# Performance work log

Hardware: AMD Instinct MI355X
Metric: run time of the kernel (lower is better)

The kernel has to match this reference:

```python
import jax, jax.numpy as jnp
import numpy as np

K_TOP = 16
TEMP = 1.0
EPS = 1e-9

def setup_inputs() -> dict:
    key = jax.random.key(0)
    k1, k2, k3 = jax.random.split(key, 3)
    B, H, N, D = 4, 8, 2048, 64
    q = jax.random.normal(k1, (B, H, N, D), dtype=jnp.float32)
    k = jax.random.normal(k2, (B, H, N, D), dtype=jnp.float32)
    u = jax.random.uniform(k3, (B, N, N), dtype=jnp.float32)
    return {"q": q, "k": k, "u": u}

def reference(q, k, u):
    # q, k: [B, H, N, D]; u: uniform noise [B, N, N]
    d_head = q.shape[-1]
    scale = 1.0 / jnp.sqrt(jnp.asarray(d_head, dtype=q.dtype))
    # [B, H, N, N] scores, then mean over heads -> [B, N, N]
    attn_scores = jnp.einsum('bhnd,bhmd->bhnm', q, k) * scale
    logits = attn_scores.mean(axis=1)
    gumbel = -jnp.log(-jnp.log(u + EPS) + EPS)
    probs = jax.nn.softmax((logits + gumbel) / TEMP, axis=-1)
    topk_vals = jax.lax.top_k(probs, K_TOP)[0]          # [B, N, K]
    thresh = topk_vals.min(axis=-1, keepdims=True)      # [B, N, 1]
    sparse_mask = (probs >= thresh).astype(probs.dtype)
    return sparse_mask[:, None, :, :]                   # [B, 1, N, N]
```

## Files before the change

### kernel.cpp

```cpp
#include <hip/hip_runtime.h>
#include <math.h>

#define BB 4
#define HH 8
#define NN 2048
#define DD 64
#define KTOP 16
#define CUT_MARGIN 1e-3f

typedef _Float16 half_t;
typedef __attribute__((ext_vector_type(8))) _Float16 half8;
typedef __attribute__((ext_vector_type(4))) _Float16 half4v;
typedef __attribute__((ext_vector_type(4))) float floatx4;

__global__ __launch_bounds__(256) void split_f16(const float* __restrict__ q,
                                                 const float* __restrict__ kk,
                                                 half_t* __restrict__ qhi,
                                                 half_t* __restrict__ qlo,
                                                 half_t* __restrict__ khi,
                                                 half_t* __restrict__ klo) {
    const int NQ4 = BB * HH * NN * DD / 4;
    int gid = blockIdx.x * 256 + threadIdx.x;
    const float* src; half_t* dhi; half_t* dlo; int i4;
    if (gid < NQ4) { src = q;  dhi = qhi; dlo = qlo; i4 = gid; }
    else           { src = kk; dhi = khi; dlo = klo; i4 = gid - NQ4; }
    float4 x = ((const float4*)src)[i4];
    float xs[4] = {x.x, x.y, x.z, x.w};
    half4v h, l;
#pragma unroll
    for (int e = 0; e < 4; ++e) {
        half_t hi = (half_t)xs[e];
        float  r  = xs[e] - (float)hi;
        h[e] = hi;
        l[e] = (half_t)(r * 2048.0f);
    }
    *(half4v*)(dhi + (size_t)i4 * 4) = h;
    *(half4v*)(dlo + (size_t)i4 * 4) = l;
}

__global__ __launch_bounds__(256, 2) void gemm_f16x3(const half_t* __restrict__ qhi,
                                                     const half_t* __restrict__ qlo,
                                                     const half_t* __restrict__ khi,
                                                     const half_t* __restrict__ klo,
                                                     float* __restrict__ L) {
    const int b  = blockIdx.z;
    const int i0 = blockIdx.y * 128;
    const int j0 = blockIdx.x * 128;
    const int tid  = threadIdx.x;
    const int wave = tid >> 6, lane = tid & 63;
    const int wr = wave >> 1, wc = wave & 1;
    const int lm = lane & 15, quad = lane >> 4;

    __shared__ __align__(16) half_t Ah[128 * 64];
    __shared__ __align__(16) half_t Al[128 * 64];
    __shared__ __align__(16) half_t Bh[128 * 64];
    __shared__ __align__(16) half_t Bl[128 * 64];

    floatx4 acc1[4][4], acc2[4][4];
#pragma unroll
    for (int tr = 0; tr < 4; ++tr)
#pragma unroll
        for (int tc = 0; tc < 4; ++tc) {
            acc1[tr][tc] = (floatx4)0.0f;
            acc2[tr][tc] = (floatx4)0.0f;
        }

    for (int h = 0; h < HH; ++h) {
        const size_t aoff = ((size_t)(b * HH + h) * NN + i0) * DD;
        const size_t boff = ((size_t)(b * HH + h) * NN + j0) * DD;
        __syncthreads();
#pragma unroll
        for (int it = 0; it < 4; ++it) {
            const int u   = it * 256 + tid;
            const int row = u >> 3;
            const int kg  = u & 7;
            const int lidx = row * 64 + ((kg ^ (row & 7)) << 3);
            const size_t ga = aoff + row * DD + kg * 8;
            const size_t gb = boff + row * DD + kg * 8;
            *(half8*)&Ah[lidx] = *(const half8*)&qhi[ga];
            *(half8*)&Al[lidx] = *(const half8*)&qlo[ga];
            *(half8*)&Bh[lidx] = *(const half8*)&khi[gb];
            *(half8*)&Bl[lidx] = *(const half8*)&klo[gb];
        }
        __syncthreads();

#pragma unroll
        for (int ks = 0; ks < 2; ++ks) {
            half8 ah[4], al[4], bh[4], bl[4];
            const int unit = ks * 4 + quad;
#pragma unroll
            for (int t = 0; t < 4; ++t) {
                const int am = wr * 64 + t * 16 + lm;
                const int bm = wc * 64 + t * 16 + lm;
                const int ai = am * 64 + ((unit ^ (am & 7)) << 3);
                const int bi = bm * 64 + ((unit ^ (bm & 7)) << 3);
                ah[t] = *(const half8*)&Ah[ai];
                al[t] = *(const half8*)&Al[ai];
                bh[t] = *(const half8*)&Bh[bi];
                bl[t] = *(const half8*)&Bl[bi];
            }
#pragma unroll
            for (int tr = 0; tr < 4; ++tr)
#pragma unroll
                for (int tc = 0; tc < 4; ++tc) {
                    acc1[tr][tc] = __builtin_amdgcn_mfma_f32_16x16x32_f16(
                        ah[tr], bh[tc], acc1[tr][tc], 0, 0, 0);
                    acc2[tr][tc] = __builtin_amdgcn_mfma_f32_16x16x32_f16(
                        ah[tr], bl[tc], acc2[tr][tc], 0, 0, 0);
                    acc2[tr][tc] = __builtin_amdgcn_mfma_f32_16x16x32_f16(
                        al[tr], bh[tc], acc2[tr][tc], 0, 0, 0);
                }
        }
    }

    const float s1 = 0.015625f;
    const float s2 = 0.015625f / 2048.0f;
#pragma unroll
    for (int tr = 0; tr < 4; ++tr)
#pragma unroll
        for (int r = 0; r < 4; ++r) {
            const int grow = i0 + wr * 64 + tr * 16 + quad * 4 + r;
            float* Lp = L + ((size_t)b * NN + grow) * NN + j0 + wc * 64 + lm;
#pragma unroll
            for (int tc = 0; tc < 4; ++tc)
                Lp[tc * 16] = acc1[tr][tc][r] * s1 + acc2[tr][tc][r] * s2;
        }
}

__device__ __forceinline__ unsigned long long flip64(double x) {
    unsigned long long v = (unsigned long long)__double_as_longlong(x);
    return v ^ ((0ULL - (v >> 63)) | 0x8000000000000000ULL);
}
__device__ __forceinline__ double unflip64(unsigned long long k) {
    unsigned long long v = (k >> 63) ? (k ^ 0x8000000000000000ULL) : ~k;
    return __longlong_as_double((long long)v);
}

__global__ __launch_bounds__(256, 3) void topk_mask(float* LM,
                                                    const float* __restrict__ u) {
    const int wave = threadIdx.x >> 6, lane = threadIdx.x & 63;
    const int row = blockIdx.x * 4 + wave;
    float* lrow = LM + (size_t)row * NN;
    const float* urow = u + (size_t)row * NN;

    __shared__ int   s_idx[4][64];
    __shared__ float s_L[4][64];

    float Lv[32], z[32];
#pragma unroll
    for (int e = 0; e < 8; ++e) {
        float4 lv = *(const float4*)(lrow + e * 256 + lane * 4);
        float4 uv = *(const float4*)(urow + e * 256 + lane * 4);
        float ls[4] = {lv.x, lv.y, lv.z, lv.w};
        float us[4] = {uv.x, uv.y, uv.z, uv.w};
#pragma unroll
        for (int s = 0; s < 4; ++s) {
            float v = (us[s] - 1.0f) + 1e-9f;
            float w = -log1pf(v);
            float g = -__logf(w + 1e-9f);
            Lv[e * 4 + s] = ls[s];
            z[e * 4 + s]  = ls[s] + g;
        }
    }

    float v = z[0];
#pragma unroll
    for (int r = 1; r < 32; ++r) v = fmaxf(v, z[r]);
#pragma unroll
    for (int kS = 2; kS <= 64; kS <<= 1) {
#pragma unroll
        for (int j = kS >> 1; j > 0; j >>= 1) {
            float o = __shfl_xor(v, j, 64);
            bool asc = ((lane & kS) == 0);
            bool lower = ((lane & j) == 0);
            float mn = fminf(v, o), mx = fmaxf(v, o);
            v = (asc == lower) ? mn : mx;
        }
    }
    const float cut = __shfl(v, 48, 64) - CUT_MARGIN;

    int c = 0;
#pragma unroll
    for (int r = 0; r < 32; ++r) {
        bool p = (z[r] >= cut);
        unsigned long long m = __ballot(p);
        if (p) {
            int slot = c + __popcll(m & ((1ULL << lane) - 1ULL));
            if (slot < 64) {
                s_idx[wave][slot] = (r >> 2) * 256 + lane * 4 + (r & 3);
                s_L[wave][slot]   = Lv[r];
            }
        }
        c += __popcll(m);
    }
    if (c > 64) c = 64;

    float4 z4 = make_float4(0.f, 0.f, 0.f, 0.f);
#pragma unroll
    for (int e = 0; e < 8; ++e)
        *(float4*)(lrow + e * 256 + lane * 4) = z4;
    __syncthreads();

    unsigned long long key = 0xFFFFFFFFFFFFFFFFULL;
    double z64 = 0.0;
    int myidx = -1;
    if (lane < c) {
        myidx = s_idx[wave][lane];
        double uu = (double)urow[myidx] + 1e-9;
        double w  = -log(uu);
        double g  = -log(w + 1e-9);
        z64 = (double)s_L[wave][lane] + g;
        key = flip64(z64);
    }
    const int rounds = c - (KTOP - 1);
    unsigned long long m = 0;
    for (int r = 0; r < rounds; ++r) {
        m = key;
#pragma unroll
        for (int off = 32; off >= 1; off >>= 1) {
            unsigned long long o = __shfl_xor(m, off, 64);
            m = (o < m) ? o : m;
        }
        unsigned long long bm = __ballot(key == m);
        if (lane == __builtin_ctzll(bm)) key = 0xFFFFFFFFFFFFFFFFULL;
    }
    double thresh = unflip64(m);
    if (myidx >= 0) lrow[myidx] = (z64 >= thresh) ? 1.0f : 0.0f;
}

extern "C" void kernel_launch(void* const* d_in, const int* in_sizes, int n_in,
                              void* d_out, int out_size, void* d_ws, size_t ws_size,
                              hipStream_t stream) {
    const float* q = (const float*)d_in[0];
    const float* k = (const float*)d_in[1];
    const float* u = (const float*)d_in[2];
    float* out = (float*)d_out;
    const size_t NQ = (size_t)BB * HH * NN * DD;
    half_t* qhi = (half_t*)d_ws;
    half_t* qlo = qhi + NQ;
    half_t* khi = qlo + NQ;
    half_t* klo = khi + NQ;

    split_f16<<<(2 * NQ / 4) / 256, 256, 0, stream>>>(q, k, qhi, qlo, khi, klo);

    dim3 grid1(NN / 128, NN / 128, BB);
    gemm_f16x3<<<grid1, 256, 0, stream>>>(qhi, qlo, khi, klo, out);

    topk_mask<<<(BB * NN) / 4, 256, 0, stream>>>(out, u);
}
```

Measured before the change: 231.0 us.

## Pre-swizzle f16 splits in global and load GEMM tiles via global_load_lds

The split kernel now writes hi/lo f16 tensors already XOR-swizzled in the LDS tile layout. The GEMM then copies each 128x64 tile straight from global memory into LDS with buffer-to-LDS direct loads, one wave per operand. This removes the register round-trip and per-element swizzle address math from the tile load. Separately, the Gumbel noise now uses a direct log of u+eps instead of log1p(u-1+eps), which is cheaper but can differ slightly in precision near u≈1.

```diff
diff --git a/kernel.cpp b/kernel.cpp
--- a/kernel.cpp
+++ b/kernel.cpp
@@ -10,32 +10,43 @@
 
 typedef _Float16 half_t;
 typedef __attribute__((ext_vector_type(8))) _Float16 half8;
-typedef __attribute__((ext_vector_type(4))) _Float16 half4v;
 typedef __attribute__((ext_vector_type(4))) float floatx4;
 
-__global__ __launch_bounds__(256) void split_f16(const float* __restrict__ q,
+__device__ __forceinline__ void gl_lds16(const half_t* g, half_t* l) {
+    __builtin_amdgcn_global_load_lds(
+        (const __attribute__((address_space(1))) void*)g,
+        (__attribute__((address_space(3))) void*)l, 16, 0, 0);
+}
+
+__global__ __launch_bounds__(256) void split_swz(const float* __restrict__ q,
                                                  const float* __restrict__ kk,
                                                  half_t* __restrict__ qhi,
                                                  half_t* __restrict__ qlo,
                                                  half_t* __restrict__ khi,
                                                  half_t* __restrict__ klo) {
-    const int NQ4 = BB * HH * NN * DD / 4;
-    int gid = blockIdx.x * 256 + threadIdx.x;
-    const float* src; half_t* dhi; half_t* dlo; int i4;
-    if (gid < NQ4) { src = q;  dhi = qhi; dlo = qlo; i4 = gid; }
-    else           { src = kk; dhi = khi; dlo = klo; i4 = gid - NQ4; }
-    float4 x = ((const float4*)src)[i4];
-    float xs[4] = {x.x, x.y, x.z, x.w};
-    half4v h, l;
-#pragma unroll
-    for (int e = 0; e < 4; ++e) {
-        half_t hi = (half_t)xs[e];
-        float  r  = xs[e] - (float)hi;
-        h[e] = hi;
-        l[e] = (half_t)(r * 2048.0f);
-    }
-    *(half4v*)(dhi + (size_t)i4 * 4) = h;
-    *(half4v*)(dlo + (size_t)i4 * 4) = l;
+    const int uidx = blockIdx.x * 256 + threadIdx.x;
+    const int row  = uidx >> 3;
+    const int kg   = uidx & 7;
+    const size_t src = (size_t)uidx * 8;
+    const size_t dst = (size_t)row * 64 + (size_t)((kg ^ (row & 7)) << 3);
+
+    float a[8], b[8];
+    *(float4*)&a[0] = *(const float4*)(q + src);
+    *(float4*)&a[4] = *(const float4*)(q + src + 4);
+    *(float4*)&b[0] = *(const float4*)(kk + src);
+    *(float4*)&b[4] = *(const float4*)(kk + src + 4);
+    half8 qh, ql, kh, kl;
+#pragma unroll
+    for (int e = 0; e < 8; ++e) {
+        half_t hq = (half_t)a[e];
+        half_t hk = (half_t)b[e];
+        qh[e] = hq; ql[e] = (half_t)((a[e] - (float)hq) * 2048.0f);
+        kh[e] = hk; kl[e] = (half_t)((b[e] - (float)hk) * 2048.0f);
+    }
+    *(half8*)(qhi + dst) = qh;
+    *(half8*)(qlo + dst) = ql;
+    *(half8*)(khi + dst) = kh;
+    *(half8*)(klo + dst) = kl;
 }
 
 __global__ __launch_bounds__(256, 2) void gemm_f16x3(const half_t* __restrict__ qhi,
@@ -47,7 +58,8 @@
     const int i0 = blockIdx.y * 128;
     const int j0 = blockIdx.x * 128;
     const int tid  = threadIdx.x;
-    const int wave = tid >> 6, lane = tid & 63;
+    const int wave = __builtin_amdgcn_readfirstlane(tid >> 6);
+    const int lane = tid & 63;
     const int wr = wave >> 1, wc = wave & 1;
     const int lm = lane & 15, quad = lane >> 4;
 
@@ -56,6 +68,8 @@
     __shared__ __align__(16) half_t Bh[128 * 64];
     __shared__ __align__(16) half_t Bl[128 * 64];
 
+    const int off0 = (lane >> 3) * 64 + (lane & 7) * 8;
+
     floatx4 acc1[4][4], acc2[4][4];
 #pragma unroll
     for (int tr = 0; tr < 4; ++tr)
@@ -68,20 +82,18 @@
     for (int h = 0; h < HH; ++h) {
         const size_t aoff = ((size_t)(b * HH + h) * NN + i0) * DD;
         const size_t boff = ((size_t)(b * HH + h) * NN + j0) * DD;
+        const half_t* gbase;
+        half_t* lbase;
+        if      (wave == 0) { gbase = qhi + aoff; lbase = Ah; }
+        else if (wave == 1) { gbase = qlo + aoff; lbase = Al; }
+        else if (wave == 2) { gbase = khi + boff; lbase = Bh; }
+        else                { gbase = klo + boff; lbase = Bl; }
+        gbase += off0;
+
         __syncthreads();
 #pragma unroll
-        for (int it = 0; it < 4; ++it) {
-            const int u   = it * 256 + tid;
-            const int row = u >> 3;
-            const int kg  = u & 7;
-            const int lidx = row * 64 + ((kg ^ (row & 7)) << 3);
-            const size_t ga = aoff + row * DD + kg * 8;
-            const size_t gb = boff + row * DD + kg * 8;
-            *(half8*)&Ah[lidx] = *(const half8*)&qhi[ga];
-            *(half8*)&Al[lidx] = *(const half8*)&qlo[ga];
-            *(half8*)&Bh[lidx] = *(const half8*)&khi[gb];
-            *(half8*)&Bl[lidx] = *(const half8*)&klo[gb];
-        }
+        for (int i = 0; i < 16; ++i)
+            gl_lds16(gbase + i * 512, lbase + i * 512);
         __syncthreads();
 
 #pragma unroll
@@ -155,8 +167,8 @@
         float us[4] = {uv.x, uv.y, uv.z, uv.w};
 #pragma unroll
         for (int s = 0; s < 4; ++s) {
-            float v = (us[s] - 1.0f) + 1e-9f;
-            float w = -log1pf(v);
+            float t = us[s] + 1e-9f;
+            float w = -__logf(t);
             float g = -__logf(w + 1e-9f);
             Lv[e * 4 + s] = ls[s];
             z[e * 4 + s]  = ls[s] + g;
@@ -241,7 +253,7 @@
     half_t* khi = qlo + NQ;
     half_t* klo = khi + NQ;
 
-    split_f16<<<(2 * NQ / 4) / 256, 256, 0, stream>>>(q, k, qhi, qlo, khi, klo);
+    split_swz<<<(int)(NQ / 8 / 256), 256, 0, stream>>>(q, k, qhi, qlo, khi, klo);
 
     dim3 grid1(NN / 128, NN / 128, BB);
     gemm_f16x3<<<grid1, 256, 0, stream>>>(qhi, qlo, khi, klo, out);
```

Result: faster. 216.7 us (-6.2%).
